# Performance work log

Measured on AMD Instinct MI355X. Metric: run time of the kernel, lower is better.

The kernel has to match this reference:

```python
import jax, jax.numpy as jnp
import numpy as np

NUM_BATCH, NUM_OBJ, NUM_DBOX, NUM_CLASSES = 64, 50, 8732, 2
JACCARD_THRESH = 0.5
NEGPOS_RATIO = 3
VARIANCE = (0.1, 0.2)


def setup_inputs() -> dict:
    key = jax.random.key(0)
    k1, k2, k3, k4, k5, k6 = jax.random.split(key, 6)
    loc_data = jax.random.normal(k1, (NUM_BATCH, NUM_DBOX, 4), dtype=jnp.float32)
    conf_data = jax.random.normal(k2, (NUM_BATCH, NUM_DBOX, NUM_CLASSES), dtype=jnp.float32)
    # default boxes in center-size form (cx, cy, w, h)
    cxcy = jax.random.uniform(k3, (NUM_DBOX, 2), minval=0.05, maxval=0.95)
    wh = jax.random.uniform(k4, (NUM_DBOX, 2), minval=0.05, maxval=0.4)
    dbox_list = jnp.concatenate([cxcy, wh], axis=1).astype(jnp.float32)
    # ground-truth boxes in point form [xmin,ymin,xmax,ymax] plus label (class 0 -> conf label 1)
    tc = jax.random.uniform(k5, (NUM_BATCH, NUM_OBJ, 2), minval=0.15, maxval=0.85)
    twh = jax.random.uniform(k6, (NUM_BATCH, NUM_OBJ, 2), minval=0.05, maxval=0.3)
    truths = jnp.concatenate([tc - twh / 2, tc + twh / 2], axis=-1)
    labels = jnp.zeros((NUM_BATCH, NUM_OBJ, 1), dtype=jnp.float32)
    targets = jnp.concatenate([truths, labels], axis=-1).astype(jnp.float32)
    return {"loc_data": loc_data, "conf_data": conf_data, "dbox_list": dbox_list, "targets": targets}


def point_form(boxes):
    # (cx,cy,w,h) -> (xmin,ymin,xmax,ymax)
    return jnp.concatenate([boxes[:, :2] - boxes[:, 2:] / 2, boxes[:, :2] + boxes[:, 2:] / 2], axis=1)


def jaccard(a, b):
    # a: [No,4], b: [Nd,4], both point form -> [No,Nd]
    lt = jnp.maximum(a[:, None, :2], b[None, :, :2])
    rb = jnp.minimum(a[:, None, 2:], b[None, :, 2:])
    wh = jnp.clip(rb - lt, 0.0)
    inter = wh[..., 0] * wh[..., 1]
    area_a = ((a[:, 2] - a[:, 0]) * (a[:, 3] - a[:, 1]))[:, None]
    area_b = ((b[:, 2] - b[:, 0]) * (b[:, 3] - b[:, 1]))[None, :]
    return inter / (area_a + area_b - inter)


def encode(matched, priors):
    # matched: [Nd,4] point form; priors: [Nd,4] center-size form
    g_cxcy = (matched[:, :2] + matched[:, 2:]) / 2 - priors[:, :2]
    g_cxcy = g_cxcy / (VARIANCE[0] * priors[:, 2:])
    g_wh = jnp.log((matched[:, 2:] - matched[:, :2]) / priors[:, 2:]) / VARIANCE[1]
    return jnp.concatenate([g_cxcy, g_wh], axis=1)


def match_one(truths, labels, dbox):
    # truths [No,4], labels [No], dbox [Nd,4] center-size
    overlaps = jaccard(truths, point_form(dbox))  # [No, Nd]
    best_prior_idx = jnp.argmax(overlaps, axis=1)          # [No]
    best_truth_overlap = jnp.max(overlaps, axis=0)          # [Nd]
    best_truth_idx = jnp.argmax(overlaps, axis=0)           # [Nd]
    best_truth_overlap = best_truth_overlap.at[best_prior_idx].set(2.0)
    best_truth_idx = best_truth_idx.at[best_prior_idx].set(jnp.arange(truths.shape[0]))
    matched = truths[best_truth_idx]                        # [Nd,4]
    conf = labels[best_truth_idx].astype(jnp.int32) + 1
    conf = jnp.where(best_truth_overlap < JACCARD_THRESH, 0, conf)
    loc = encode(matched, dbox)
    return loc, conf


def smooth_l1(x, t):
    d = jnp.abs(x - t)
    return jnp.where(d < 1.0, 0.5 * d * d, d - 0.5)


def cross_entropy(logits, labels):
    # logits [..., C], labels [...] int -> elementwise CE
    logp = jax.nn.log_softmax(logits, axis=-1)
    return -jnp.take_along_axis(logp, labels[..., None], axis=-1)[..., 0]


def reference(loc_data, conf_data, dbox_list, targets):
    num_batch, num_dbox, _ = loc_data.shape
    truths = targets[..., :-1]        # [B,No,4]
    labels = targets[..., -1]          # [B,No]
    loc_t, conf_t_label = jax.vmap(match_one, in_axes=(0, 0, None))(truths, labels, dbox_list)
    pos_mask = conf_t_label > 0        # [B,Nd]

    # localization loss: smooth L1 over positive priors, mean over selected elements
    l1 = smooth_l1(loc_data, loc_t)                               # [B,Nd,4]
    n_pos_elems = 4.0 * jnp.sum(pos_mask)
    loss_l = jnp.nan_to_num(jnp.sum(l1 * pos_mask[..., None]) / n_pos_elems)

    # per-prior confidence loss for hard-negative mining
    ce = cross_entropy(conf_data, conf_t_label)                   # [B,Nd]
    ce_mined = jnp.where(pos_mask, 0.0, ce)
    loss_idx = jnp.argsort(-ce_mined, axis=1)                     # descending sort
    idx_rank = jnp.argsort(loss_idx, axis=1)
    num_pos = jnp.sum(pos_mask, axis=1, keepdims=True)            # [B,1]
    num_neg = jnp.clip(num_pos * NEGPOS_RATIO, 20, num_dbox)
    neg_mask = idx_rank < num_neg                                 # [B,Nd]

    posf = pos_mask.astype(ce.dtype)
    negf = neg_mask.astype(ce.dtype)
    loss_c_pos = jnp.nan_to_num(jnp.sum(ce * posf) / jnp.sum(posf))
    loss_c_neg = jnp.nan_to_num(jnp.sum(ce * negf) / jnp.sum(negf))
    loss_c = loss_c_pos + loss_c_neg
    return jnp.stack([loss_l, loss_c, loss_c_pos, loss_c_neg])
```

## Files before the change

kernel.cpp:

```cpp
#include <hip/hip_runtime.h>

#define NB     64
#define NOBJ   50
#define ND     8732
#define BLK    256
#define NW     (BLK/64)
#define PPT    4
#define PRB    (BLK*PPT)
#define NBA    9
#define TB     13
#define GRID   (NB*NBA + NB*TB)
#define TILE   1024
#define NTILE  ((ND + TILE - 1)/TILE)
#define BLK2   1024
#define NW2    (BLK2/64)
#define ITER2  ((ND+BLK2-1)/BLK2)
#define ND4    (ND/4)

__device__ float              g_part[NB*5];
__device__ float4             g_ce4[(size_t)NB*ND4];
__device__ unsigned long long g_keys[NB*NOBJ];
__device__ int                g_hist[(size_t)NB*NBA*256];
__device__ float              g_bp[NB*NBA*3];
__device__ int                g_done;

__device__ __forceinline__ float iou_rn(float px1,float py1,float px2,float py2,float pa,
                                        float tx1,float ty1,float tx2,float ty2,float ta){
    float ltx=fmaxf(tx1,px1), lty=fmaxf(ty1,py1);
    float rbx=fminf(tx2,px2), rby=fminf(ty2,py2);
    float ww=fmaxf(__fsub_rn(rbx,ltx),0.f), hh=fmaxf(__fsub_rn(rby,lty),0.f);
    float inter=__fmul_rn(ww,hh);
    return __fdividef(inter, __fsub_rn(__fadd_rn(ta,pa),inter));
}
__device__ __forceinline__ float lse2(float x0,float x1){
    float m=fmaxf(x0,x1);
    return m+__logf(__expf(x0-m)+__expf(x1-m));
}
__device__ __forceinline__ float sl1_enc(float4 p,float tx1,float ty1,float tx2,float ty2,float4 ld){
    float g0=((tx1+tx2)*0.5f-p.x)/(0.1f*p.z);
    float g1=((ty1+ty2)*0.5f-p.y)/(0.1f*p.w);
    float g2=__logf((tx2-tx1)/p.z)*5.0f;
    float g3=__logf((ty2-ty1)/p.w)*5.0f;
    float t0=fabsf(ld.x-g0),t1=fabsf(ld.y-g1),t2=fabsf(ld.z-g2),t3=fabsf(ld.w-g3);
    return (t0<1.f?0.5f*t0*t0:t0-0.5f)+(t1<1.f?0.5f*t1*t1:t1-0.5f)
          +(t2<1.f?0.5f*t2*t2:t2-0.5f)+(t3<1.f?0.5f*t3*t3:t3-0.5f);
}

__global__ __launch_bounds__(BLK) void k1(const float* __restrict__ loc_data,
                                          const float* __restrict__ conf_data,
                                          const float* __restrict__ dbox,
                                          const float* __restrict__ targets){
    __shared__ float s_tx1[NOBJ],s_ty1[NOBJ],s_tx2[NOBJ],s_ty2[NOBJ],s_lab[NOBJ];
    __shared__ int   s_wh[NW*256];
    __shared__ float s_r1[NW],s_r2[NW],s_r3[NW];
    __shared__ float s_px1[TILE],s_py1[TILE],s_px2[TILE],s_py2[TILE],s_pa[TILE];

    const int blk=blockIdx.x, tid=threadIdx.x, lane=tid&63, wv=tid>>6;
    const float4* dbox4=reinterpret_cast<const float4*>(dbox);
    if (blk==0 && tid==0) g_done=0;

    if (blk < NB*NBA) {
        const int b=blk/NBA, spl=blk%NBA;
        if (tid<NOBJ){
            const float* t=targets+(b*NOBJ+tid)*5;
            s_tx1[tid]=t[0];s_ty1[tid]=t[1];s_tx2[tid]=t[2];s_ty2[tid]=t[3];s_lab[tid]=t[4];
        }
        for (int i=tid;i<NW*256;i+=BLK) s_wh[i]=0;
        __syncthreads();

        const int d0=spl*PRB;
        const bool vld=(d0+tid*PPT)<ND;
        float px1[PPT],py1[PPT],px2[PPT],py2[PPT],pa[PPT];
        float bov[PPT]; int bj[PPT];
#pragma unroll
        for (int q=0;q<PPT;++q){
            bov[q]=-1.f; bj[q]=0;
            px1[q]=py1[q]=px2[q]=py2[q]=pa[q]=0.f;
            if (vld){
                float4 p=dbox4[d0+tid*PPT+q];
                float hw=__fmul_rn(0.5f,p.z), hh=__fmul_rn(0.5f,p.w);
                px1[q]=__fsub_rn(p.x,hw); py1[q]=__fsub_rn(p.y,hh);
                px2[q]=__fadd_rn(p.x,hw); py2[q]=__fadd_rn(p.y,hh);
                pa[q]=__fmul_rn(p.z,p.w);
            }
        }
        const float* tg=targets+(size_t)b*NOBJ*5;
        for (int c=0;c<5;++c){
            float tx1c[10],ty1c[10],tx2c[10],ty2c[10],tac[10];
#pragma unroll
            for (int jj=0;jj<10;++jj){
                int j=c*10+jj;
                tx1c[jj]=tg[j*5+0]; ty1c[jj]=tg[j*5+1];
                tx2c[jj]=tg[j*5+2]; ty2c[jj]=tg[j*5+3];
                tac[jj]=__fmul_rn(__fsub_rn(tx2c[jj],tx1c[jj]),__fsub_rn(ty2c[jj],ty1c[jj]));
            }
#pragma unroll
            for (int q=0;q<PPT;++q){
#pragma unroll
                for (int jj=0;jj<10;++jj){
                    float iou=iou_rn(px1[q],py1[q],px2[q],py2[q],pa[q],
                                     tx1c[jj],ty1c[jj],tx2c[jj],ty2c[jj],tac[jj]);
                    if (iou>bov[q]){bov[q]=iou;bj[q]=c*10+jj;}
                }
            }
        }
        float np=0.f,sl=0.f,sc=0.f;
        if (vld){
            const size_t cbase=((size_t)b*ND+d0)/2;
            float4 cfa=reinterpret_cast<const float4*>(conf_data)[cbase+tid*2];
            float4 cfb=reinterpret_cast<const float4*>(conf_data)[cbase+tid*2+1];
            float raw[PPT];
#pragma unroll
            for (int q=0;q<PPT;++q){
                const int d=d0+tid*PPT+q;
                float cfx=(q==0)?cfa.x:(q==1)?cfa.z:(q==2)?cfb.x:cfb.z;
                float cfy=(q==0)?cfa.y:(q==1)?cfa.w:(q==2)?cfb.y:cfb.w;
                float l=lse2(cfx,cfy);
                bool pos=!(bov[q]<0.5f);
                int jb=bj[q];
                int lab=pos?((int)s_lab[jb]+1):0;
                float cev=l-(lab>=1?cfy:cfx);
                raw[q]=pos?-cev:cev;
                atomicAdd(&s_wh[wv*256+(int)(__float_as_uint(fmaxf(raw[q],0.f))>>24)],1);
                if (pos){
                    np+=1.f; sc+=cev;
                    float4 p=dbox4[d];
                    float4 ldv=reinterpret_cast<const float4*>(loc_data)[(size_t)b*ND+d];
                    sl+=sl1_enc(p,s_tx1[jb],s_ty1[jb],s_tx2[jb],s_ty2[jb],ldv);
                }
            }
            float4 st; st.x=raw[0];st.y=raw[1];st.z=raw[2];st.w=raw[3];
            g_ce4[((size_t)b*ND+d0)/4+tid]=st;
        }
#pragma unroll
        for (int off=32;off>=1;off>>=1){
            np+=__shfl_xor(np,off,64); sl+=__shfl_xor(sl,off,64); sc+=__shfl_xor(sc,off,64);
        }
        if (lane==0){s_r1[wv]=np;s_r2[wv]=sl;s_r3[wv]=sc;}
        __syncthreads();
        if (tid==0){
            float a=0.f,bb=0.f,cc=0.f;
            for (int w=0;w<NW;++w){a+=s_r1[w];bb+=s_r2[w];cc+=s_r3[w];}
            g_bp[(b*NBA+spl)*3+0]=a;
            g_bp[(b*NBA+spl)*3+1]=bb;
            g_bp[(b*NBA+spl)*3+2]=cc;
        }
        if (tid<256){
            int s=0;
            for (int w=0;w<NW;++w) s+=s_wh[w*256+tid];
            g_hist[(size_t)(b*NBA+spl)*256+tid]=s;
        }
    } else {
        const int r=blk-NB*NBA;
        const int b=r/TB;
        const int t=(r%TB)*NW+wv;
        const bool tv=t<NOBJ;
        float tx1=0,ty1=0,tx2=0,ty2=0,ta=1.f;
        if (tv){
            const float* tt=targets+(b*NOBJ+t)*5;
            tx1=tt[0];ty1=tt[1];tx2=tt[2];ty2=tt[3];
            ta=__fmul_rn(__fsub_rn(tx2,tx1),__fsub_rn(ty2,ty1));
        }
        float bt=-1.f; int bd=0;
        for (int tile=0;tile<NTILE;++tile){
            const int base=tile*TILE;
#pragma unroll
            for (int i=0;i<TILE/BLK;++i){
                int dl=tid+i*BLK;
                int d=base+dl;
                float4 p=make_float4(0.f,0.f,0.f,0.f);
                if (d<ND) p=dbox4[d];
                float hw=__fmul_rn(0.5f,p.z), hh=__fmul_rn(0.5f,p.w);
                s_px1[dl]=__fsub_rn(p.x,hw); s_py1[dl]=__fsub_rn(p.y,hh);
                s_px2[dl]=__fadd_rn(p.x,hw); s_py2[dl]=__fadd_rn(p.y,hh);
                s_pa[dl]=__fmul_rn(p.z,p.w);
            }
            __syncthreads();
            if (tv){
#pragma unroll 4
                for (int dd=lane;dd<TILE;dd+=64){
                    float iou=iou_rn(s_px1[dd],s_py1[dd],s_px2[dd],s_py2[dd],s_pa[dd],
                                     tx1,ty1,tx2,ty2,ta);
                    if (iou>bt){bt=iou;bd=base+dd;}
                }
            }
            __syncthreads();
        }
        if (tv){
            unsigned long long key=((unsigned long long)__float_as_uint(bt)<<32)
                                  |(unsigned long long)(0xFFFFFFFFu-(unsigned)bd);
#pragma unroll
            for (int off=32;off>=1;off>>=1){
                unsigned long long o=__shfl_xor(key,off,64);
                if (o>key) key=o;
            }
            if (lane==0) g_keys[b*NOBJ+t]=key;
        }
    }
}

__global__ __launch_bounds__(BLK2) void k2(const float* __restrict__ loc_data,
                                           const float* __restrict__ conf_data,
                                           const float* __restrict__ dbox,
                                           const float* __restrict__ targets,
                                           float* __restrict__ out){
    __shared__ float4 s_ce4[ND4];
    __shared__ unsigned int s_dj[NOBJ];
    __shared__ float s_tx1[NOBJ],s_ty1[NOBJ],s_tx2[NOBJ],s_ty2[NOBJ],s_ta[NOBJ],s_lab[NOBJ];
    __shared__ int   s_hist[256];
    __shared__ int   s_wh[NW2*256];
    __shared__ float s_bpl[NBA*3];
    __shared__ float s_rf[NW2]; __shared__ int s_ri[NW2];
    __shared__ int   s_wt[4];
    __shared__ float s_dnp,s_dsl,s_dsc;
    __shared__ int   s_sel,s_krem,s_kk,s_last;
    float* s_ce=(float*)s_ce4;

    const int b=blockIdx.x, tid=threadIdx.x, lane=tid&63, wv=tid>>6;

    if (tid<NOBJ){
        const float* t=targets+(b*NOBJ+tid)*5;
        float x1=t[0],y1=t[1],x2=t[2],y2=t[3];
        s_tx1[tid]=x1;s_ty1[tid]=y1;s_tx2[tid]=x2;s_ty2[tid]=y2;
        s_ta[tid]=__fmul_rn(__fsub_rn(x2,x1),__fsub_rn(y2,y1));
        s_lab[tid]=t[4];
        s_dj[tid]=0xFFFFFFFFu-(unsigned)(g_keys[b*NOBJ+tid]&0xFFFFFFFFull);
    }
    for (int i=tid;i<ND4;i+=BLK2) s_ce4[i]=g_ce4[(size_t)b*ND4+i];
    if (tid<256){
        int s=0;
        for (int sp=0;sp<NBA;++sp) s+=g_hist[(size_t)(b*NBA+sp)*256+tid];
        s_hist[tid]=s;
    }
    if (tid<NBA*3) s_bpl[tid]=g_bp[b*NBA*3+tid];
    __syncthreads();

    float dnp=0.f,dsl=0.f,dsc=0.f;
    if (tid<NOBJ){
        unsigned d=s_dj[tid]; bool win=true;
        for (int j2=tid+1;j2<NOBJ;++j2) if (s_dj[j2]==d){win=false;break;}
        if (win){
            float4 p=reinterpret_cast<const float4*>(dbox)[d];
            float hw=__fmul_rn(0.5f,p.z), hh2=__fmul_rn(0.5f,p.w);
            float ppx1=__fsub_rn(p.x,hw),ppy1=__fsub_rn(p.y,hh2);
            float ppx2=__fadd_rn(p.x,hw),ppy2=__fadd_rn(p.y,hh2);
            float ppa=__fmul_rn(p.z,p.w);
            float bov=-1.f; int jb=0;
            for (int j=0;j<NOBJ;++j){
                float iou=iou_rn(ppx1,ppy1,ppx2,ppy2,ppa,
                                 s_tx1[j],s_ty1[j],s_tx2[j],s_ty2[j],s_ta[j]);
                if (iou>bov){bov=iou;jb=j;}
            }
            bool oldpos=!(bov<0.5f);
            float2 cf=reinterpret_cast<const float2*>(conf_data)[(size_t)b*ND+d];
            float l=lse2(cf.x,cf.y);
            float4 ldv=reinterpret_cast<const float4*>(loc_data)[(size_t)b*ND+d];
            int labN=(int)s_lab[tid]+1;
            float ceN=l-(labN>=1?cf.y:cf.x);
            dsc+=ceN; dsl+=sl1_enc(p,s_tx1[tid],s_ty1[tid],s_tx2[tid],s_ty2[tid],ldv);
            if (oldpos){
                int labO=(int)s_lab[jb]+1;
                float ceO=l-(labO>=1?cf.y:cf.x);
                dsc-=ceO; dsl-=sl1_enc(p,s_tx1[jb],s_ty1[jb],s_tx2[jb],s_ty2[jb],ldv);
            } else dnp+=1.f;
            float oldraw=s_ce[d];
            atomicAdd(&s_hist[(int)(__float_as_uint(fmaxf(oldraw,0.f))>>24)],-1);
            atomicAdd(&s_hist[0],1);
            s_ce[d]=-ceN;
        }
    }
    if (wv==0){
#pragma unroll
        for (int off=32;off>=1;off>>=1){
            dnp+=__shfl_xor(dnp,off,64); dsl+=__shfl_xor(dsl,off,64); dsc+=__shfl_xor(dsc,off,64);
        }
        if (lane==0){s_dnp=dnp;s_dsl=dsl;s_dsc=dsc;}
    }
    __syncthreads();
    if (tid==0){
        float np=s_dnp, sl=s_dsl, sc=s_dsc;
        for (int i=0;i<NBA;++i){np+=s_bpl[i*3];sl+=s_bpl[i*3+1];sc+=s_bpl[i*3+2];}
        int npi=(int)np; int k=npi*3; if(k<20)k=20; if(k>ND)k=ND;
        s_kk=k;
        g_part[b*5+0]=np; g_part[b*5+1]=sl; g_part[b*5+2]=sc; g_part[b*5+3]=(float)k;
    }
    __syncthreads();
    const int k=s_kk;

    unsigned prefix=0u,pmask=0u; int krem=k;
    for (int p=0;p<3;++p){
        const int shift=24-p*8;
        int cnt=0;
        if (p==0){
            if (tid<256) cnt=s_hist[tid];
        } else {
            for (int i=tid;i<NW2*256;i+=BLK2) s_wh[i]=0;
            __syncthreads();
            for (int it=0;it<ITER2;++it){
                int d=tid+it*BLK2;
                if (d<ND){
                    unsigned vb=__float_as_uint(fmaxf(s_ce[d],0.f));
                    if ((vb&pmask)==prefix)
                        atomicAdd(&s_wh[wv*256+(int)((vb>>shift)&255u)],1);
                }
            }
            __syncthreads();
            if (tid<256){
                for (int w=0;w<NW2;++w) cnt+=s_wh[w*256+tid];
            }
        }
        int S=cnt,add=0;
        if (tid<256){
#pragma unroll
            for (int off=1;off<64;off<<=1){
                int t=__shfl_down(S,off,64);
                if (lane+off<64) S+=t;
            }
            if (lane==0) s_wt[wv]=S;
        }
        __syncthreads();
        if (tid<256){
            for (int w=wv+1;w<4;++w) add+=s_wt[w];
            S+=add;
            int Snext=__shfl_down(S,1,64);
            if (lane==63) Snext=add;
            if (S>=krem && Snext<krem){s_sel=tid;s_krem=krem-(S-cnt);}
        }
        __syncthreads();
        prefix|=((unsigned)s_sel)<<shift;
        pmask|=255u<<shift;
        krem=s_krem;
        __syncthreads();
    }
    const float T=__uint_as_float(prefix);

    int cgt=0; float sgt=0.f;
    for (int it=0;it<ITER2;++it){
        int d=tid+it*BLK2;
        if (d<ND){
            float v=fmaxf(s_ce[d],0.f);
            if (v>T){cgt++;sgt+=v;}
        }
    }
#pragma unroll
    for (int off=32;off>=1;off>>=1){cgt+=__shfl_xor(cgt,off,64);sgt+=__shfl_xor(sgt,off,64);}
    if (lane==0){s_ri[wv]=cgt;s_rf[wv]=sgt;}
    __syncthreads();
    if (tid==0){
        int cg=0; float sg=0.f;
        for (int w=0;w<NW2;++w){cg+=s_ri[w];sg+=s_rf[w];}
        int need=k-cg;
        float stk=sg+(float)need*T;
        if (!(T>0.f)&&need>0){
            int taken=0;
            for (int d=0;d<ND&&taken<need;++d){
                float r2=s_ce[d];
                if (!(r2>0.f)){stk+=fabsf(r2);++taken;}
            }
        }
        g_part[b*5+4]=stk;
    }

    if (tid==0){__threadfence(); int old=atomicAdd(&g_done,1); s_last=(old==NB-1)?1:0;}
    __syncthreads();
    if (s_last&&tid<NB){
        __threadfence();
        volatile float* gp=g_part;
        float np=gp[tid*5+0],sl=gp[tid*5+1],sc=gp[tid*5+2],kk=gp[tid*5+3],st=gp[tid*5+4];
#pragma unroll
        for (int off=32;off>=1;off>>=1){
            np+=__shfl_xor(np,off,64);sl+=__shfl_xor(sl,off,64);
            sc+=__shfl_xor(sc,off,64);kk+=__shfl_xor(kk,off,64);st+=__shfl_xor(st,off,64);
        }
        if (tid==0){
            float loss_l=(np>0.f)?sl/(4.f*np):0.f;
            float lcp=(np>0.f)?sc/np:0.f;
            float lcn=(kk>0.f)?st/kk:0.f;
            out[0]=loss_l;out[1]=lcp+lcn;out[2]=lcp;out[3]=lcn;
        }
    }
}

extern "C" void kernel_launch(void* const* d_in, const int* in_sizes, int n_in,
                              void* d_out, int out_size, void* d_ws, size_t ws_size,
                              hipStream_t stream) {
    const float* loc     = (const float*)d_in[0];
    const float* conf    = (const float*)d_in[1];
    const float* dboxp   = (const float*)d_in[2];
    const float* targets = (const float*)d_in[3];
    float* out = (float*)d_out;

    k1<<<GRID, BLK, 0, stream>>>(loc, conf, dboxp, targets);
    k2<<<NB, BLK2, 0, stream>>>(loc, conf, dboxp, targets, out);
}
```

Before: 143.5 us.

## Fuse per-truth best-prior search into per-prior IoU pass with division-free compares

Removes the separate block group that re-scanned all priors per truth object. The per-truth best prior is now tracked inside the existing per-prior IoU loop and reduced with wave shuffles, per-wave shared slots and a per-block partial key, and k2 merges those partial keys. IoU comparisons use cross-multiplied intersection/denominator pairs instead of a division per pair, dividing once at the end. This drops roughly half the grid and the duplicate IoU work, at the cost of more registers and reductions in k1 and possible tie or rounding differences from the cross-multiply compare.

```diff
diff --git a/kernel.cpp b/kernel.cpp
--- a/kernel.cpp
+++ b/kernel.cpp
@@ -8,10 +8,8 @@
 #define PPT    4
 #define PRB    (BLK*PPT)
 #define NBA    9
-#define TB     13
-#define GRID   (NB*NBA + NB*TB)
-#define TILE   1024
-#define NTILE  ((ND + TILE - 1)/TILE)
+#define CH     10
+#define NCH    5
 #define BLK2   1024
 #define NW2    (BLK2/64)
 #define ITER2  ((ND+BLK2-1)/BLK2)
@@ -19,18 +17,22 @@
 
 __device__ float              g_part[NB*5];
 __device__ float4             g_ce4[(size_t)NB*ND4];
-__device__ unsigned long long g_keys[NB*NOBJ];
+__device__ unsigned long long g_kpart[NB*NBA*NOBJ];
 __device__ int                g_hist[(size_t)NB*NBA*256];
 __device__ float              g_bp[NB*NBA*3];
 __device__ int                g_done;
 
-__device__ __forceinline__ float iou_rn(float px1,float py1,float px2,float py2,float pa,
-                                        float tx1,float ty1,float tx2,float ty2,float ta){
+__device__ __forceinline__ void iou_parts(float px1,float py1,float px2,float py2,float pa,
+                                          float tx1,float ty1,float tx2,float ty2,float ta,
+                                          float& inter,float& den){
     float ltx=fmaxf(tx1,px1), lty=fmaxf(ty1,py1);
     float rbx=fminf(tx2,px2), rby=fminf(ty2,py2);
     float ww=fmaxf(__fsub_rn(rbx,ltx),0.f), hh=fmaxf(__fsub_rn(rby,lty),0.f);
-    float inter=__fmul_rn(ww,hh);
-    return __fdividef(inter, __fsub_rn(__fadd_rn(ta,pa),inter));
+    inter=__fmul_rn(ww,hh);
+    den=__fsub_rn(__fadd_rn(ta,pa),inter);
+}
+__device__ __forceinline__ bool better(float iN,float dN,float iO,float dO){
+    return __fmul_rn(iN,dO) > __fmul_rn(iO,dN);
 }
 __device__ __forceinline__ float lse2(float x0,float x1){
     float m=fmaxf(x0,x1);
@@ -51,151 +53,138 @@
                                           const float* __restrict__ dbox,
                                           const float* __restrict__ targets){
     __shared__ float s_tx1[NOBJ],s_ty1[NOBJ],s_tx2[NOBJ],s_ty2[NOBJ],s_lab[NOBJ];
+    __shared__ unsigned long long s_wk[NW][NOBJ];
     __shared__ int   s_wh[NW*256];
     __shared__ float s_r1[NW],s_r2[NW],s_r3[NW];
-    __shared__ float s_px1[TILE],s_py1[TILE],s_px2[TILE],s_py2[TILE],s_pa[TILE];
-
-    const int blk=blockIdx.x, tid=threadIdx.x, lane=tid&63, wv=tid>>6;
+
+    const int blk=blockIdx.x, b=blk/NBA, spl=blk%NBA;
+    const int tid=threadIdx.x, lane=tid&63, wv=tid>>6;
     const float4* dbox4=reinterpret_cast<const float4*>(dbox);
     if (blk==0 && tid==0) g_done=0;
 
-    if (blk < NB*NBA) {
-        const int b=blk/NBA, spl=blk%NBA;
-        if (tid<NOBJ){
-            const float* t=targets+(b*NOBJ+tid)*5;
-            s_tx1[tid]=t[0];s_ty1[tid]=t[1];s_tx2[tid]=t[2];s_ty2[tid]=t[3];s_lab[tid]=t[4];
-        }
-        for (int i=tid;i<NW*256;i+=BLK) s_wh[i]=0;
-        __syncthreads();
-
-        const int d0=spl*PRB;
-        const bool vld=(d0+tid*PPT)<ND;
-        float px1[PPT],py1[PPT],px2[PPT],py2[PPT],pa[PPT];
-        float bov[PPT]; int bj[PPT];
-#pragma unroll
-        for (int q=0;q<PPT;++q){
-            bov[q]=-1.f; bj[q]=0;
-            px1[q]=py1[q]=px2[q]=py2[q]=pa[q]=0.f;
-            if (vld){
-                float4 p=dbox4[d0+tid*PPT+q];
-                float hw=__fmul_rn(0.5f,p.z), hh=__fmul_rn(0.5f,p.w);
-                px1[q]=__fsub_rn(p.x,hw); py1[q]=__fsub_rn(p.y,hh);
-                px2[q]=__fadd_rn(p.x,hw); py2[q]=__fadd_rn(p.y,hh);
-                pa[q]=__fmul_rn(p.z,p.w);
-            }
-        }
-        const float* tg=targets+(size_t)b*NOBJ*5;
-        for (int c=0;c<5;++c){
-            float tx1c[10],ty1c[10],tx2c[10],ty2c[10],tac[10];
-#pragma unroll
-            for (int jj=0;jj<10;++jj){
-                int j=c*10+jj;
-                tx1c[jj]=tg[j*5+0]; ty1c[jj]=tg[j*5+1];
-                tx2c[jj]=tg[j*5+2]; ty2c[jj]=tg[j*5+3];
-                tac[jj]=__fmul_rn(__fsub_rn(tx2c[jj],tx1c[jj]),__fsub_rn(ty2c[jj],ty1c[jj]));
-            }
-#pragma unroll
-            for (int q=0;q<PPT;++q){
-#pragma unroll
-                for (int jj=0;jj<10;++jj){
-                    float iou=iou_rn(px1[q],py1[q],px2[q],py2[q],pa[q],
-                                     tx1c[jj],ty1c[jj],tx2c[jj],ty2c[jj],tac[jj]);
-                    if (iou>bov[q]){bov[q]=iou;bj[q]=c*10+jj;}
-                }
-            }
-        }
-        float np=0.f,sl=0.f,sc=0.f;
+    if (tid<NOBJ){
+        const float* t=targets+(b*NOBJ+tid)*5;
+        s_tx1[tid]=t[0];s_ty1[tid]=t[1];s_tx2[tid]=t[2];s_ty2[tid]=t[3];s_lab[tid]=t[4];
+    }
+    for (int i=tid;i<NW*256;i+=BLK) s_wh[i]=0;
+    __syncthreads();
+
+    const int d0=spl*PRB;
+    const bool vld=(d0+tid*PPT)<ND;
+    float px1[PPT],py1[PPT],px2[PPT],py2[PPT],pa[PPT];
+    float ibest[PPT],dbest[PPT]; int bj[PPT];
+#pragma unroll
+    for (int q=0;q<PPT;++q){
+        ibest[q]=-1.f; dbest[q]=1.f; bj[q]=0;
+        px1[q]=py1[q]=px2[q]=py2[q]=pa[q]=0.f;
         if (vld){
-            const size_t cbase=((size_t)b*ND+d0)/2;
-            float4 cfa=reinterpret_cast<const float4*>(conf_data)[cbase+tid*2];
-            float4 cfb=reinterpret_cast<const float4*>(conf_data)[cbase+tid*2+1];
-            float raw[PPT];
+            float4 p=dbox4[d0+tid*PPT+q];
+            float hw=__fmul_rn(0.5f,p.z), hh=__fmul_rn(0.5f,p.w);
+            px1[q]=__fsub_rn(p.x,hw); py1[q]=__fsub_rn(p.y,hh);
+            px2[q]=__fadd_rn(p.x,hw); py2[q]=__fadd_rn(p.y,hh);
+            pa[q]=__fmul_rn(p.z,p.w);
+        }
+    }
+
+    const float* tg=targets+(size_t)b*NOBJ*5;
+#pragma unroll 1
+    for (int c=0;c<NCH;++c){
+        float tx1c[CH],ty1c[CH],tx2c[CH],ty2c[CH],tac[CH];
+#pragma unroll
+        for (int jj=0;jj<CH;++jj){
+            int j=c*CH+jj;
+            tx1c[jj]=tg[j*5+0]; ty1c[jj]=tg[j*5+1];
+            tx2c[jj]=tg[j*5+2]; ty2c[jj]=tg[j*5+3];
+            tac[jj]=__fmul_rn(__fsub_rn(tx2c[jj],tx1c[jj]),__fsub_rn(ty2c[jj],ty1c[jj]));
+        }
+        float tiN[CH],tdN[CH]; int tdd[CH];
+#pragma unroll
+        for (int jj=0;jj<CH;++jj){tiN[jj]=-1.f;tdN[jj]=1.f;tdd[jj]=0;}
+
+        if (vld){
 #pragma unroll
             for (int q=0;q<PPT;++q){
                 const int d=d0+tid*PPT+q;
-                float cfx=(q==0)?cfa.x:(q==1)?cfa.z:(q==2)?cfb.x:cfb.z;
-                float cfy=(q==0)?cfa.y:(q==1)?cfa.w:(q==2)?cfb.y:cfb.w;
-                float l=lse2(cfx,cfy);
-                bool pos=!(bov[q]<0.5f);
-                int jb=bj[q];
-                int lab=pos?((int)s_lab[jb]+1):0;
-                float cev=l-(lab>=1?cfy:cfx);
-                raw[q]=pos?-cev:cev;
-                atomicAdd(&s_wh[wv*256+(int)(__float_as_uint(fmaxf(raw[q],0.f))>>24)],1);
-                if (pos){
-                    np+=1.f; sc+=cev;
-                    float4 p=dbox4[d];
-                    float4 ldv=reinterpret_cast<const float4*>(loc_data)[(size_t)b*ND+d];
-                    sl+=sl1_enc(p,s_tx1[jb],s_ty1[jb],s_tx2[jb],s_ty2[jb],ldv);
+#pragma unroll
+                for (int jj=0;jj<CH;++jj){
+                    float inter,den;
+                    iou_parts(px1[q],py1[q],px2[q],py2[q],pa[q],
+                              tx1c[jj],ty1c[jj],tx2c[jj],ty2c[jj],tac[jj],inter,den);
+                    if (better(inter,den,ibest[q],dbest[q])){ibest[q]=inter;dbest[q]=den;bj[q]=c*CH+jj;}
+                    if (better(inter,den,tiN[jj],tdN[jj])){tiN[jj]=inter;tdN[jj]=den;tdd[jj]=d;}
                 }
             }
-            float4 st; st.x=raw[0];st.y=raw[1];st.z=raw[2];st.w=raw[3];
-            g_ce4[((size_t)b*ND+d0)/4+tid]=st;
-        }
-#pragma unroll
-        for (int off=32;off>=1;off>>=1){
-            np+=__shfl_xor(np,off,64); sl+=__shfl_xor(sl,off,64); sc+=__shfl_xor(sc,off,64);
-        }
-        if (lane==0){s_r1[wv]=np;s_r2[wv]=sl;s_r3[wv]=sc;}
-        __syncthreads();
-        if (tid==0){
-            float a=0.f,bb=0.f,cc=0.f;
-            for (int w=0;w<NW;++w){a+=s_r1[w];bb+=s_r2[w];cc+=s_r3[w];}
-            g_bp[(b*NBA+spl)*3+0]=a;
-            g_bp[(b*NBA+spl)*3+1]=bb;
-            g_bp[(b*NBA+spl)*3+2]=cc;
-        }
-        if (tid<256){
-            int s=0;
-            for (int w=0;w<NW;++w) s+=s_wh[w*256+tid];
-            g_hist[(size_t)(b*NBA+spl)*256+tid]=s;
-        }
-    } else {
-        const int r=blk-NB*NBA;
-        const int b=r/TB;
-        const int t=(r%TB)*NW+wv;
-        const bool tv=t<NOBJ;
-        float tx1=0,ty1=0,tx2=0,ty2=0,ta=1.f;
-        if (tv){
-            const float* tt=targets+(b*NOBJ+t)*5;
-            tx1=tt[0];ty1=tt[1];tx2=tt[2];ty2=tt[3];
-            ta=__fmul_rn(__fsub_rn(tx2,tx1),__fsub_rn(ty2,ty1));
-        }
-        float bt=-1.f; int bd=0;
-        for (int tile=0;tile<NTILE;++tile){
-            const int base=tile*TILE;
-#pragma unroll
-            for (int i=0;i<TILE/BLK;++i){
-                int dl=tid+i*BLK;
-                int d=base+dl;
-                float4 p=make_float4(0.f,0.f,0.f,0.f);
-                if (d<ND) p=dbox4[d];
-                float hw=__fmul_rn(0.5f,p.z), hh=__fmul_rn(0.5f,p.w);
-                s_px1[dl]=__fsub_rn(p.x,hw); s_py1[dl]=__fsub_rn(p.y,hh);
-                s_px2[dl]=__fadd_rn(p.x,hw); s_py2[dl]=__fadd_rn(p.y,hh);
-                s_pa[dl]=__fmul_rn(p.z,p.w);
-            }
-            __syncthreads();
-            if (tv){
-#pragma unroll 4
-                for (int dd=lane;dd<TILE;dd+=64){
-                    float iou=iou_rn(s_px1[dd],s_py1[dd],s_px2[dd],s_py2[dd],s_pa[dd],
-                                     tx1,ty1,tx2,ty2,ta);
-                    if (iou>bt){bt=iou;bd=base+dd;}
-                }
-            }
-            __syncthreads();
-        }
-        if (tv){
-            unsigned long long key=((unsigned long long)__float_as_uint(bt)<<32)
-                                  |(unsigned long long)(0xFFFFFFFFu-(unsigned)bd);
-#pragma unroll
-            for (int off=32;off>=1;off>>=1){
-                unsigned long long o=__shfl_xor(key,off,64);
-                if (o>key) key=o;
-            }
-            if (lane==0) g_keys[b*NOBJ+t]=key;
-        }
+        }
+#pragma unroll
+        for (int jj=0;jj<CH;++jj){
+            float tbv=tiN[jj]/tdN[jj];
+            float m=tbv;
+#pragma unroll
+            for (int off=32;off>=1;off>>=1) m=fmaxf(m,__shfl_xor(m,off,64));
+            unsigned long long msk=__ballot(tbv==m);
+            int lead=__builtin_ctzll(msk);
+            int dwin=__shfl(tdd[jj],lead,64);
+            if (lane==0){
+                s_wk[wv][c*CH+jj]=(m>=0.f)
+                    ?(((unsigned long long)__float_as_uint(m)<<32)
+                      |(unsigned long long)(0xFFFFFFFFu-(unsigned)dwin))
+                    :0ull;
+            }
+        }
+    }
+    __syncthreads();
+    if (tid<NOBJ){
+        unsigned long long m=s_wk[0][tid];
+        for (int w=1;w<NW;++w){unsigned long long o=s_wk[w][tid]; if(o>m)m=o;}
+        g_kpart[((size_t)b*NBA+spl)*NOBJ+tid]=m;
+    }
+
+    float np=0.f,sl=0.f,sc=0.f;
+    if (vld){
+        const size_t cbase=((size_t)b*ND+d0)/2;
+        float4 cfa=reinterpret_cast<const float4*>(conf_data)[cbase+tid*2];
+        float4 cfb=reinterpret_cast<const float4*>(conf_data)[cbase+tid*2+1];
+        float raw[PPT];
+#pragma unroll
+        for (int q=0;q<PPT;++q){
+            const int d=d0+tid*PPT+q;
+            float cfx=(q==0)?cfa.x:(q==1)?cfa.z:(q==2)?cfb.x:cfb.z;
+            float cfy=(q==0)?cfa.y:(q==1)?cfa.w:(q==2)?cfb.y:cfb.w;
+            float l=lse2(cfx,cfy);
+            float bovq=ibest[q]/dbest[q];
+            bool pos=!(bovq<0.5f);
+            int jb=bj[q];
+            int lab=pos?((int)s_lab[jb]+1):0;
+            float cev=l-(lab>=1?cfy:cfx);
+            raw[q]=pos?-cev:cev;
+            atomicAdd(&s_wh[wv*256+(int)(__float_as_uint(fmaxf(raw[q],0.f))>>24)],1);
+            if (pos){
+                np+=1.f; sc+=cev;
+                float4 p=dbox4[d];
+                float4 ldv=reinterpret_cast<const float4*>(loc_data)[(size_t)b*ND+d];
+                sl+=sl1_enc(p,s_tx1[jb],s_ty1[jb],s_tx2[jb],s_ty2[jb],ldv);
+            }
+        }
+        float4 st; st.x=raw[0];st.y=raw[1];st.z=raw[2];st.w=raw[3];
+        g_ce4[((size_t)b*ND+d0)/4+tid]=st;
+    }
+#pragma unroll
+    for (int off=32;off>=1;off>>=1){
+        np+=__shfl_xor(np,off,64); sl+=__shfl_xor(sl,off,64); sc+=__shfl_xor(sc,off,64);
+    }
+    if (lane==0){s_r1[wv]=np;s_r2[wv]=sl;s_r3[wv]=sc;}
+    __syncthreads();
+    if (tid==0){
+        float a=0.f,bb=0.f,cc=0.f;
+        for (int w=0;w<NW;++w){a+=s_r1[w];bb+=s_r2[w];cc+=s_r3[w];}
+        g_bp[(b*NBA+spl)*3+0]=a;
+        g_bp[(b*NBA+spl)*3+1]=bb;
+        g_bp[(b*NBA+spl)*3+2]=cc;
+    }
+    if (tid<256){
+        int s=0;
+        for (int w=0;w<NW;++w) s+=s_wh[w*256+tid];
+        g_hist[(size_t)(b*NBA+spl)*256+tid]=s;
     }
 }
 
@@ -205,6 +194,7 @@
                                            const float* __restrict__ targets,
                                            float* __restrict__ out){
     __shared__ float4 s_ce4[ND4];
+    __shared__ unsigned long long s_kmm[NOBJ*NBA];
     __shared__ unsigned int s_dj[NOBJ];
     __shared__ float s_tx1[NOBJ],s_ty1[NOBJ],s_tx2[NOBJ],s_ty2[NOBJ],s_ta[NOBJ],s_lab[NOBJ];
     __shared__ int   s_hist[256];
@@ -224,7 +214,10 @@
         s_tx1[tid]=x1;s_ty1[tid]=y1;s_tx2[tid]=x2;s_ty2[tid]=y2;
         s_ta[tid]=__fmul_rn(__fsub_rn(x2,x1),__fsub_rn(y2,y1));
         s_lab[tid]=t[4];
-        s_dj[tid]=0xFFFFFFFFu-(unsigned)(g_keys[b*NOBJ+tid]&0xFFFFFFFFull);
+    }
+    if (tid<NOBJ*NBA){
+        int j=tid/NBA, s=tid-j*NBA;
+        s_kmm[tid]=g_kpart[((size_t)b*NBA+s)*NOBJ+j];
     }
     for (int i=tid;i<ND4;i+=BLK2) s_ce4[i]=g_ce4[(size_t)b*ND4+i];
     if (tid<256){
@@ -233,6 +226,12 @@
         s_hist[tid]=s;
     }
     if (tid<NBA*3) s_bpl[tid]=g_bp[b*NBA*3+tid];
+    __syncthreads();
+    if (tid<NOBJ){
+        unsigned long long m=s_kmm[tid*NBA];
+        for (int s=1;s<NBA;++s){unsigned long long o=s_kmm[tid*NBA+s]; if(o>m)m=o;}
+        s_dj[tid]=0xFFFFFFFFu-(unsigned)(m&0xFFFFFFFFull);
+    }
     __syncthreads();
 
     float dnp=0.f,dsl=0.f,dsc=0.f;
@@ -245,12 +244,14 @@
             float ppx1=__fsub_rn(p.x,hw),ppy1=__fsub_rn(p.y,hh2);
             float ppx2=__fadd_rn(p.x,hw),ppy2=__fadd_rn(p.y,hh2);
             float ppa=__fmul_rn(p.z,p.w);
-            float bov=-1.f; int jb=0;
+            float ib=-1.f,db=1.f; int jb=0;
             for (int j=0;j<NOBJ;++j){
-                float iou=iou_rn(ppx1,ppy1,ppx2,ppy2,ppa,
-                                 s_tx1[j],s_ty1[j],s_tx2[j],s_ty2[j],s_ta[j]);
-                if (iou>bov){bov=iou;jb=j;}
-            }
+                float inter,den;
+                iou_parts(ppx1,ppy1,ppx2,ppy2,ppa,
+                          s_tx1[j],s_ty1[j],s_tx2[j],s_ty2[j],s_ta[j],inter,den);
+                if (better(inter,den,ib,db)){ib=inter;db=den;jb=j;}
+            }
+            float bov=ib/db;
             bool oldpos=!(bov<0.5f);
             float2 cf=reinterpret_cast<const float2*>(conf_data)[(size_t)b*ND+d];
             float l=lse2(cf.x,cf.y);
@@ -390,6 +391,6 @@
     const float* targets = (const float*)d_in[3];
     float* out = (float*)d_out;
 
-    k1<<<GRID, BLK, 0, stream>>>(loc, conf, dboxp, targets);
+    k1<<<NB*NBA, BLK, 0, stream>>>(loc, conf, dboxp, targets);
     k2<<<NB, BLK2, 0, stream>>>(loc, conf, dboxp, targets, out);
 }
```

After: 149.7 us. 1.04x slower.
